# Kernel optimization log

Hardware: AMD Instinct MI355X
Metric: run time of the kernel (lower is better)

## Reference

```python
import jax, jax.numpy as jnp
import numpy as np

EMBED = 768
HEADS = 12
HEAD_DIM = EMBED // HEADS  # 64
NUM_CLS = 1
WIN = 16        # one-sided window radius
DIL = 4         # dilation
THETA = 10000.0
COORD_HIGH = 100000.0


def _rotate_half(x):
    # [..., x1, x2, ...] -> [..., -x2, x1, ...] over adjacent pairs
    x1 = x[..., 0::2]
    x2 = x[..., 1::2]
    return jnp.stack([-x2, x1], axis=-1).reshape(x.shape)


def _rope2d(x, coords):
    # x: (B, H, L, head_dim); coords: (B, L, 2) pixel coords
    half = HEAD_DIM // 2
    inv_freq = 1.0 / THETA ** (jnp.arange(0, half, 2, dtype=jnp.float32) / half)  # (half/2,)
    xy = coords.astype(jnp.float32) / COORD_HIGH
    fx = xy[..., 0:1] * inv_freq  # (B, L, half/2)
    fy = xy[..., 1:2] * inv_freq
    fx = jnp.repeat(fx, 2, axis=-1)  # (B, L, half)
    fy = jnp.repeat(fy, 2, axis=-1)
    freqs = jnp.concatenate([fx, fy], axis=-1)  # (B, L, head_dim)
    cos = jnp.cos(freqs)[:, None]  # (B, 1, L, head_dim)
    sin = jnp.sin(freqs)[:, None]
    return x * cos + _rotate_half(x) * sin


def setup_inputs() -> dict:
    key = jax.random.key(0)
    ks = jax.random.split(key, 5)
    B, L = 1, 4096
    S = L + NUM_CLS
    x = jax.random.normal(ks[0], (B, S, EMBED), jnp.float32)
    coords = jax.random.randint(ks[1], (B, L, 2), 0, 100000).astype(jnp.int32)
    qkv_w = jax.random.normal(ks[2], (3 * EMBED, EMBED), jnp.float32) * 0.02
    qkv_b = jnp.zeros((3 * EMBED,), jnp.float32)
    out_w = jax.random.normal(ks[3], (EMBED, EMBED), jnp.float32) * 0.02
    out_b = jnp.zeros((EMBED,), jnp.float32)
    return {"x": x, "coords": coords, "qkv_w": qkv_w, "qkv_b": qkv_b,
            "out_w": out_w, "out_b": out_b}


def reference(x, coords, qkv_w, qkv_b, out_w, out_b):
    B, S, E = x.shape
    L = S - NUM_CLS
    # QKV projection -> (3, B, H, S, hd)
    qkv = (x @ qkv_w.T + qkv_b).reshape(B, S, 3, HEADS, HEAD_DIM)
    qkv = qkv.transpose(2, 0, 3, 1, 4)
    q, k, v = qkv[0], qkv[1], qkv[2]
    # 2D RoPE on patch tokens only
    q = jnp.concatenate([q[:, :, :NUM_CLS], _rope2d(q[:, :, NUM_CLS:], coords)], axis=2)
    k = jnp.concatenate([k[:, :, :NUM_CLS], _rope2d(k[:, :, NUM_CLS:], coords)], axis=2)
    scale = 1.0 / np.sqrt(HEAD_DIM).astype(np.float32)

    q_cls, k_cls, v_cls = q[:, :, :NUM_CLS], k[:, :, :NUM_CLS], v[:, :, :NUM_CLS]
    q_p, k_p, v_p = q[:, :, NUM_CLS:], k[:, :, NUM_CLS:], v[:, :, NUM_CLS:]

    # CLS (global) queries attend to everything
    cls_scores = jnp.einsum('bhqd,bhkd->bhqk', q_cls, k) * scale
    cls_out = jnp.einsum('bhqk,bhkd->bhqd', jax.nn.softmax(cls_scores, axis=-1), v)

    # Patch queries: single softmax over [CLS keys | dilated local window]
    win_len = 2 * WIN + 1
    pos = jnp.arange(L)
    rel = (jnp.arange(win_len) - WIN) * DIL
    key_idx = pos[:, None] + rel[None, :]          # (L, W) absolute patch key index
    valid = (key_idx >= 0) & (key_idx < L)         # boundary patches: masked, not wrapped
    gidx = jnp.clip(key_idx, 0, L - 1)
    k_win = jnp.take(k_p, gidx, axis=2)            # (B, H, L, W, hd)
    v_win = jnp.take(v_p, gidx, axis=2)
    s_win = jnp.einsum('bhld,bhlwd->bhlw', q_p, k_win) * scale
    s_win = jnp.where(valid[None, None], s_win, -jnp.inf)
    s_cls = jnp.einsum('bhld,bhcd->bhlc', q_p, k_cls) * scale
    attn = jax.nn.softmax(jnp.concatenate([s_cls, s_win], axis=-1), axis=-1)
    a_cls, a_win = attn[..., :NUM_CLS], attn[..., NUM_CLS:]
    patch_out = (jnp.einsum('bhlc,bhcd->bhld', a_cls, v_cls)
                 + jnp.einsum('bhlw,bhlwd->bhld', a_win, v_win))

    out = jnp.concatenate([cls_out, patch_out], axis=2)   # (B, H, S, hd)
    out = out.transpose(0, 2, 1, 3).reshape(B, S, E)
    return out @ out_w.T + out_b
```

## Files before the change

kernel.cpp:

```cpp
#include <hip/hip_runtime.h>
#include <hip/hip_bf16.h>

namespace {

constexpr int kS = 4097;
constexpr int kL = 4096;
constexpr int kE = 768;
constexpr int kH = 12;
constexpr int kD = 64;
constexpr int kQKVN = 2304;
constexpr int kT = 1024;
constexpr int kClsChunks = 32;
constexpr int kClsStride = 68;
constexpr float kScale = 0.125f;

typedef short short8 __attribute__((ext_vector_type(8)));
typedef short short4v __attribute__((ext_vector_type(4)));
typedef float f32x4 __attribute__((ext_vector_type(4)));

__device__ inline short f2bf(float x) {
  __hip_bfloat16 b = __float2bfloat16(x);
  return *reinterpret_cast<short*>(&b);
}
__device__ inline float bf2f(short u) {
  unsigned int x = ((unsigned int)(unsigned short)u) << 16;
  union { unsigned int u32; float f; } c;
  c.u32 = x;
  return c.f;
}

__device__ inline void store_c(float* p, float v) { *p = v; }
__device__ inline void store_c(short* p, float v) { *p = f2bf(v); }

__device__ inline int xcd_swz(int bid, int nwg) {
  const int q = nwg >> 3, r = nwg & 7;
  const int x = bid & 7, o = bid >> 3;
  return (x < r ? x * (q + 1) : r * (q + 1) + (x - r) * q) + o;
}

#define GLOAD_LDS16(g, l)                                                        \
  __builtin_amdgcn_global_load_lds(                                              \
      (const __attribute__((address_space(1))) unsigned int*)(g),                \
      (__attribute__((address_space(3))) unsigned int*)(l), 16, 0, 0)

__global__ __launch_bounds__(256) void cvt3_kernel(const float* __restrict__ x,
                                                   const float* __restrict__ w,
                                                   const float* __restrict__ ow,
                                                   short* __restrict__ xb,
                                                   short* __restrict__ wb,
                                                   short* __restrict__ owb,
                                                   int n4x, int n4w, int n4o) {
  const int total = n4x + n4w + n4o;
  int i = blockIdx.x * blockDim.x + threadIdx.x;
  const int stride = gridDim.x * blockDim.x;
  for (; i < total; i += stride) {
    const float* src;
    short* dst;
    int k;
    if (i < n4x) { src = x; dst = xb; k = i; }
    else if (i < n4x + n4w) { src = w; dst = wb; k = i - n4x; }
    else { src = ow; dst = owb; k = i - n4x - n4w; }
    f32x4 v = reinterpret_cast<const f32x4*>(src)[k];
    short4v o;
#pragma unroll
    for (int j = 0; j < 4; ++j) o[j] = f2bf(v[j]);
    reinterpret_cast<short4v*>(dst)[k] = o;
  }
}

template <bool ROPE, typename TC>
__global__ __launch_bounds__(256) void gemm_tile_kernel(const short* __restrict__ A,
                                                        const short* __restrict__ W,
                                                        const float* __restrict__ bias,
                                                        TC* __restrict__ C,
                                                        int Mreal, int N, int K, int ntm,
                                                        const int* __restrict__ coords) {
  __shared__ short Ash[2][64 * 64];
  __shared__ short Bsh[2][128 * 64];
  const int nwg = gridDim.x;
  const int wid = xcd_swz(blockIdx.x, nwg);
  const int m0 = (wid % ntm) * 64;
  const int n0 = (wid / ntm) * 128;
  const int t = threadIdx.x;
  const int lane = t & 63;
  const int wave = t >> 6;
  const int wr = wave >> 1, wc = wave & 1;
  const int lrow = lane & 15;
  const int lgrp = lane >> 4;

  const int srow = t >> 3;
  const int scol = ((t & 7) ^ (srow & 7)) << 3;
  int ar0 = m0 + srow;       if (ar0 > Mreal - 1) ar0 = Mreal - 1;
  int ar1 = m0 + 32 + srow;  if (ar1 > Mreal - 1) ar1 = Mreal - 1;
  const int br0 = n0 + srow, br1 = n0 + 32 + srow;
  const int br2 = n0 + 64 + srow, br3 = n0 + 96 + srow;

#define STAGE(buf, k0)                                                  \
  do {                                                                  \
    GLOAD_LDS16(A + (size_t)ar0 * K + (k0) + scol, &Ash[buf][t * 8]);   \
    GLOAD_LDS16(A + (size_t)ar1 * K + (k0) + scol, &Ash[buf][2048 + t * 8]); \
    GLOAD_LDS16(W + (size_t)br0 * K + (k0) + scol, &Bsh[buf][t * 8]);   \
    GLOAD_LDS16(W + (size_t)br1 * K + (k0) + scol, &Bsh[buf][2048 + t * 8]); \
    GLOAD_LDS16(W + (size_t)br2 * K + (k0) + scol, &Bsh[buf][4096 + t * 8]); \
    GLOAD_LDS16(W + (size_t)br3 * K + (k0) + scol, &Bsh[buf][6144 + t * 8]); \
  } while (0)

  f32x4 acc[2][4] = {};
  const int nsteps = K / 64;

  STAGE(0, 0);
  __syncthreads();

  int cur = 0;
  for (int tt = 0; tt < nsteps; ++tt) {
    if (tt + 1 < nsteps) STAGE(cur ^ 1, (tt + 1) * 64);

#pragma unroll
    for (int ks = 0; ks < 2; ++ks) {
      short8 a[2], b[4];
#pragma unroll
      for (int mi = 0; mi < 2; ++mi) {
        const int row = wr * 32 + mi * 16 + lrow;
        const int ch = (ks * 4 + lgrp) ^ (row & 7);
        a[mi] = *reinterpret_cast<const short8*>(&Ash[cur][row * 64 + ch * 8]);
      }
#pragma unroll
      for (int ni = 0; ni < 4; ++ni) {
        const int row = wc * 64 + ni * 16 + lrow;
        const int ch = (ks * 4 + lgrp) ^ (row & 7);
        b[ni] = *reinterpret_cast<const short8*>(&Bsh[cur][row * 64 + ch * 8]);
      }
#pragma unroll
      for (int mi = 0; mi < 2; ++mi)
#pragma unroll
        for (int ni = 0; ni < 4; ++ni)
          acc[mi][ni] = __builtin_amdgcn_mfma_f32_16x16x32_bf16(a[mi], b[ni], acc[mi][ni], 0, 0, 0);
    }

    __syncthreads();
    cur ^= 1;
  }
#undef STAGE

  const int rg = lgrp << 2;
  for (int ni = 0; ni < 4; ++ni) {
    const int col = n0 + wc * 64 + ni * 16 + lrow;
    const float bz = bias[col];
    const int sec = col / 768;
    const int dh = col & 63;
    const bool odd = dh & 1;
    const int jf = (dh >> 1) & 15;
    const bool usex = (dh >> 1) < 16;
    const float invf = __powf(10000.0f, -(float)jf * (1.0f / 16.0f));
    for (int mi = 0; mi < 2; ++mi) {
      const int rowb = m0 + wr * 32 + mi * 16 + rg;
#pragma unroll
      for (int r = 0; r < 4; ++r) {
        const int row = rowb + r;
        float v = acc[mi][ni][r] + bz;
        if (ROPE && sec != 2) {
          const float partner = __shfl_xor(v, 1);
          float cs = 1.f, sn = 0.f;
          if (row > 0) {
            const int cl = min(row, kS - 1) - 1;
            const float cx = (float)coords[cl * 2] * 1e-5f;
            const float cy = (float)coords[cl * 2 + 1] * 1e-5f;
            __sincosf((usex ? cx : cy) * invf, &sn, &cs);
          }
          v = odd ? (v * cs + partner * sn) : (v * cs - partner * sn);
          if (sec == 0) v *= kScale;
        }
        if (row < Mreal) store_c(&C[(size_t)row * N + col], v);
      }
    }
  }
}

__global__ __launch_bounds__(256) void attn_kernel(const short* __restrict__ qkv,
                                                   short* __restrict__ attn,
                                                   float* __restrict__ part) {
  __shared__ short Pl[4][32][104];
  __shared__ float sm[4], sl[4], sa[4][64];
  const int lane = threadIdx.x & 63;
  const int wv = threadIdx.x >> 6;

  if (blockIdx.x >= 384) {
    const int idx = blockIdx.x - 384;
    const int h = idx >> 5;
    const int c = idx & 31;
    const int start = c * 128;
    const int end = (c == kClsChunks - 1) ? kS : start + 128;
    const float qd = bf2f(qkv[h * kD + lane]);
    float m = -INFINITY, lsum = 0.f, acc = 0.f;
    for (int s = start + wv; s < end; s += 4) {
      float tt = qd * bf2f(qkv[(size_t)s * kQKVN + kE + h * kD + lane]);
      tt += __shfl_xor(tt, 1); tt += __shfl_xor(tt, 2); tt += __shfl_xor(tt, 4);
      tt += __shfl_xor(tt, 8); tt += __shfl_xor(tt, 16); tt += __shfl_xor(tt, 32);
      const float vd = bf2f(qkv[(size_t)s * kQKVN + 2 * kE + h * kD + lane]);
      const float mnew = fmaxf(m, tt);
      const float cor = __expf(m - mnew);
      const float p = __expf(tt - mnew);
      lsum = lsum * cor + p;
      acc = acc * cor + p * vd;
      m = mnew;
    }
    sa[wv][lane] = acc;
    if (lane == 0) { sm[wv] = m; sl[wv] = lsum; }
    __syncthreads();
    if (wv == 0) {
      float M = fmaxf(fmaxf(sm[0], sm[1]), fmaxf(sm[2], sm[3]));
      float Lt = 0.f, Av = 0.f;
#pragma unroll
      for (int w = 0; w < 4; ++w) {
        const float cw = __expf(sm[w] - M);
        Lt += sl[w] * cw;
        Av += sa[w][lane] * cw;
      }
      float* p = part + ((size_t)h * kClsChunks + c) * kClsStride;
      p[lane] = Av;
      if (lane == 0) { p[64] = M; p[65] = Lt; }
    }
    return;
  }

  const int unit = blockIdx.x * 4 + wv;
  const int t0 = (unit & 31) * 32;
  const int res = (unit >> 5) & 3;
  const int h = unit >> 7;
  const int lrow = lane & 15;
  const int lgrp = lane >> 4;
  const int kg = lgrp * 8;
  const int rg = lgrp * 4;

  f32x4 s_acc[2][4] = {};
  f32x4 s_cls[2] = {};
  short8 aq[2][2];
#pragma unroll
  for (int mi = 0; mi < 2; ++mi) {
    const int tq = t0 + mi * 16 + lrow;
    const size_t row = (size_t)(4 * tq + res + 1) * kQKVN + h * kD;
#pragma unroll
    for (int ks = 0; ks < 2; ++ks)
      aq[mi][ks] = *reinterpret_cast<const short8*>(qkv + row + ks * 32 + kg);
  }
#pragma unroll
  for (int ni = 0; ni < 4; ++ni) {
    int u = t0 - 16 + ni * 16 + lrow;
    u = min(max(u, 0), kT - 1);
    const size_t row = (size_t)(4 * u + res + 1) * kQKVN + kE + h * kD;
    short8 bk[2];
#pragma unroll
    for (int ks = 0; ks < 2; ++ks)
      bk[ks] = *reinterpret_cast<const short8*>(qkv + row + ks * 32 + kg);
#pragma unroll
    for (int mi = 0; mi < 2; ++mi)
#pragma unroll
      for (int ks = 0; ks < 2; ++ks)
        s_acc[mi][ni] = __builtin_amdgcn_mfma_f32_16x16x32_bf16(aq[mi][ks], bk[ks], s_acc[mi][ni], 0, 0, 0);
  }
  {
    short8 bc[2] = {};
    if (lrow == 0) {
#pragma unroll
      for (int ks = 0; ks < 2; ++ks)
        bc[ks] = *reinterpret_cast<const short8*>(qkv + kE + h * kD + ks * 32 + kg);
    }
#pragma unroll
    for (int mi = 0; mi < 2; ++mi)
#pragma unroll
      for (int ks = 0; ks < 2; ++ks)
        s_cls[mi] = __builtin_amdgcn_mfma_f32_16x16x32_bf16(aq[mi][ks], bc[ks], s_cls[mi], 0, 0, 0);
  }

#pragma unroll
  for (int i = 0; i < 2; ++i) {
    const int idx = i * 64 + lane;
    const int q = idx >> 2, ch = idx & 3;
    short8 z = {};
    *reinterpret_cast<short8*>(&Pl[wv][q][64 + ch * 8]) = z;
  }

#pragma unroll
  for (int mi = 0; mi < 2; ++mi) {
#pragma unroll
    for (int r = 0; r < 4; ++r) {
      const int q = mi * 16 + rg + r;
      float sw[4];
      float m = -INFINITY;
#pragma unroll
      for (int ni = 0; ni < 4; ++ni) {
        const int kk = ni * 16 + lrow;
        const int u = t0 - 16 + kk;
        const bool valid = (kk >= q) & (kk <= q + 32) & (u >= 0) & (u < kT);
        sw[ni] = valid ? s_acc[mi][ni][r] : -INFINITY;
        m = fmaxf(m, sw[ni]);
      }
      float scl = (lrow == 0) ? s_cls[mi][r] : -INFINITY;
      m = fmaxf(m, scl);
      m = fmaxf(m, __shfl_xor(m, 1)); m = fmaxf(m, __shfl_xor(m, 2));
      m = fmaxf(m, __shfl_xor(m, 4)); m = fmaxf(m, __shfl_xor(m, 8));
      float lsum = 0.f, ps[4];
#pragma unroll
      for (int ni = 0; ni < 4; ++ni) { ps[ni] = __expf(sw[ni] - m); lsum += ps[ni]; }
      const float pc = __expf(scl - m);
      lsum += pc;
      lsum += __shfl_xor(lsum, 1); lsum += __shfl_xor(lsum, 2);
      lsum += __shfl_xor(lsum, 4); lsum += __shfl_xor(lsum, 8);
      const float inv = __builtin_amdgcn_rcpf(lsum);
#pragma unroll
      for (int ni = 0; ni < 4; ++ni) Pl[wv][q][ni * 16 + lrow] = f2bf(ps[ni] * inv);
      if (lrow == 0) Pl[wv][q][64] = f2bf(pc * inv);
    }
  }

  f32x4 o_acc[4][2] = {};
#pragma unroll
  for (int ks = 0; ks < 3; ++ks) {
    short8 bp[2];
#pragma unroll
    for (int nq = 0; nq < 2; ++nq)
      bp[nq] = *reinterpret_cast<const short8*>(&Pl[wv][nq * 16 + lrow][ks * 32 + kg]);
    short8 av[4];
#pragma unroll
    for (int md = 0; md < 4; ++md) {
      if (ks < 2) {
        const int d = md * 16 + lrow;
#pragma unroll
        for (int e = 0; e < 8; ++e) {
          const int kk = ks * 32 + kg + e;
          int u = t0 - 16 + kk;
          u = min(max(u, 0), kT - 1);
          av[md][e] = qkv[(size_t)(4 * u + res + 1) * kQKVN + 2 * kE + h * kD + d];
        }
      } else {
        short8 z = {};
        av[md] = z;
        if (lgrp == 0)
          av[md][0] = qkv[2 * kE + h * kD + md * 16 + lrow];
      }
#pragma unroll
      for (int nq = 0; nq < 2; ++nq)
        o_acc[md][nq] = __builtin_amdgcn_mfma_f32_16x16x32_bf16(av[md], bp[nq], o_acc[md][nq], 0, 0, 0);
    }
  }

#pragma unroll
  for (int md = 0; md < 4; ++md)
#pragma unroll
    for (int nq = 0; nq < 2; ++nq)
#pragma unroll
      for (int r = 0; r < 4; ++r) {
        const int d = md * 16 + rg + r;
        const int q = nq * 16 + lrow;
        const int s = 4 * (t0 + q) + res + 1;
        attn[(size_t)s * kE + h * kD + d] = f2bf(o_acc[md][nq][r]);
      }
}

__global__ __launch_bounds__(64) void cls_combine_kernel(const float* __restrict__ part,
                                                         short* __restrict__ attn) {
  const int h = blockIdx.x;
  const int lane = threadIdx.x;
  float mc[kClsChunks], lc[kClsChunks], ac[kClsChunks];
#pragma unroll
  for (int c = 0; c < kClsChunks; ++c) {
    const float* p = part + ((size_t)h * kClsChunks + c) * kClsStride;
    mc[c] = p[64];
    lc[c] = p[65];
    ac[c] = p[lane];
  }
  float M = -INFINITY;
#pragma unroll
  for (int c = 0; c < kClsChunks; ++c) M = fmaxf(M, mc[c]);
  float L = 0.f, A = 0.f;
#pragma unroll
  for (int c = 0; c < kClsChunks; ++c) {
    const float w = __expf(mc[c] - M);
    L += lc[c] * w;
    A += ac[c] * w;
  }
  attn[h * kD + lane] = f2bf(A / L);
}

}

extern "C" void kernel_launch(void* const* d_in, const int* in_sizes, int n_in,
                              void* d_out, int out_size, void* d_ws, size_t ws_size,
                              hipStream_t stream) {
  const float* x = (const float*)d_in[0];
  const int* coords = (const int*)d_in[1];
  const float* qkv_w = (const float*)d_in[2];
  const float* qkv_b = (const float*)d_in[3];
  const float* out_w = (const float*)d_in[4];
  const float* out_b = (const float*)d_in[5];
  float* out = (float*)d_out;

  char* p = (char*)d_ws;
  short* qkvb = (short*)p;                p += (size_t)kS * kQKVN * sizeof(short);
  short* xb = (short*)p;                  p += (size_t)kS * kE * sizeof(short);
  short* wb = (short*)p;                  p += (size_t)kQKVN * kE * sizeof(short);
  short* owb = (short*)p;                 p += (size_t)kE * kE * sizeof(short);
  short* attnb = (short*)p;               p += (size_t)kS * kE * sizeof(short);
  float* clsp = (float*)p;

  const int n4x = kS * kE / 4;
  const int n4w = kQKVN * kE / 4;
  const int n4o = kE * kE / 4;
  cvt3_kernel<<<2048, 256, 0, stream>>>(x, qkv_w, out_w, xb, wb, owb, n4x, n4w, n4o);

  gemm_tile_kernel<true, short><<<1170, 256, 0, stream>>>(xb, wb, qkv_b, qkvb, kS, kQKVN, kE, 65, coords);
  attn_kernel<<<768, 256, 0, stream>>>(qkvb, attnb, clsp);
  cls_combine_kernel<<<kH, 64, 0, stream>>>(clsp, attnb);
  gemm_tile_kernel<false, float><<<390, 256, 0, stream>>>(attnb, owb, out_b, out, kS, kE, kE, 65, nullptr);
}
```

Measured before the change: 95.67 us.

## Replace QKV GEMM with 256x256-tile 8-wave kernel using phased LDS pipelining

Adds a new QKV projection GEMM kernel with 256x256 tiles, 512 threads, and double-buffered, split-half LDS staging. It interleaves global-to-LDS loads with MFMA phases under explicit barriers and raised priority. The larger tile increases data reuse and cuts the workgroup count from 1170 to 153. The trade-offs are fewer workgroups than the machine's compute units, padding waste on M, and a heavier RoPE epilogue per thread. The loop count is hard-coded to K=768.

Result: slower. 114.0 us (+19.2%).

```diff
diff --git a/kernel.cpp b/kernel.cpp
--- a/kernel.cpp
+++ b/kernel.cpp
@@ -69,6 +69,185 @@
 }
 
 template <bool ROPE, typename TC>
+__global__ __launch_bounds__(512, 2) void gemm_8ph_kernel(const short* __restrict__ A,
+                                                          const short* __restrict__ W,
+                                                          const float* __restrict__ bias,
+                                                          TC* __restrict__ C,
+                                                          int Mreal, int N, int K, int ntm,
+                                                          const int* __restrict__ coords) {
+  __shared__ short Ash[2][2][128 * 64];
+  __shared__ short Bsh[2][2][128 * 64];
+  const int nwg = gridDim.x;
+  const int wid = xcd_swz(blockIdx.x, nwg);
+  const int m0 = (wid % ntm) * 256;
+  const int n0 = (wid / ntm) * 256;
+  const int t = threadIdx.x;
+  const int lane = t & 63;
+  const int wave = t >> 6;
+  const int wm = wave >> 2;
+  const int wn = wave & 3;
+  const int lrow = lane & 15;
+  const int lgrp = lane >> 4;
+
+  int srow[2], scol[2];
+#pragma unroll
+  for (int j = 0; j < 2; ++j) {
+    const int c = j * 512 + t;
+    srow[j] = c >> 3;
+    scol[j] = ((c & 7) ^ (srow[j] & 7)) << 3;
+  }
+
+#define STAGEA(kt, h)                                                         \
+  do {                                                                        \
+    _Pragma("unroll") for (int j = 0; j < 2; ++j) {                           \
+      int gr = m0 + (h) * 128 + srow[j];                                      \
+      if (gr > Mreal - 1) gr = Mreal - 1;                                     \
+      GLOAD_LDS16(A + (size_t)gr * K + (kt) * 64 + scol[j],                   \
+                  &Ash[(kt) & 1][h][(j * 512 + t) * 8]);                      \
+    }                                                                         \
+  } while (0)
+#define STAGEB(kt, h)                                                         \
+  do {                                                                        \
+    _Pragma("unroll") for (int j = 0; j < 2; ++j) {                           \
+      const int gr = n0 + (h) * 128 + srow[j];                                \
+      GLOAD_LDS16(W + (size_t)gr * K + (kt) * 64 + scol[j],                   \
+                  &Bsh[(kt) & 1][h][(j * 512 + t) * 8]);                      \
+    }                                                                         \
+  } while (0)
+
+  short8 breg[4][2], areg[2][2];
+#define READB(buf)                                                            \
+  do {                                                                        \
+    _Pragma("unroll") for (int nf = 0; nf < 4; ++nf)                          \
+      _Pragma("unroll") for (int ks = 0; ks < 2; ++ks) {                      \
+        const int rowh = (wn & 1) * 64 + nf * 16 + lrow;                      \
+        const int ch = (ks * 4 + lgrp) ^ (rowh & 7);                          \
+        breg[nf][ks] = *reinterpret_cast<const short8*>(                      \
+            &Bsh[buf][wn >> 1][rowh * 64 + ch * 8]);                          \
+      }                                                                       \
+  } while (0)
+#define READA(buf, p)                                                         \
+  do {                                                                        \
+    _Pragma("unroll") for (int mi = 0; mi < 2; ++mi)                          \
+      _Pragma("unroll") for (int ks = 0; ks < 2; ++ks) {                      \
+        const int rowh = ((p) * 2 + mi) * 16 + lrow;                          \
+        const int ch = (ks * 4 + lgrp) ^ (rowh & 7);                          \
+        areg[mi][ks] = *reinterpret_cast<const short8*>(                      \
+            &Ash[buf][wm][rowh * 64 + ch * 8]);                               \
+      }                                                                       \
+  } while (0)
+#define MFMA16(p)                                                             \
+  do {                                                                        \
+    _Pragma("unroll") for (int mi = 0; mi < 2; ++mi)                          \
+      _Pragma("unroll") for (int nf = 0; nf < 4; ++nf)                        \
+        _Pragma("unroll") for (int ks = 0; ks < 2; ++ks)                      \
+          acc[(p) * 2 + mi][nf] = __builtin_amdgcn_mfma_f32_16x16x32_bf16(    \
+              areg[mi][ks], breg[nf][ks], acc[(p) * 2 + mi][nf], 0, 0, 0);    \
+  } while (0)
+#define WAIT_LGKM0                                                            \
+  do {                                                                        \
+    asm volatile("s_waitcnt lgkmcnt(0)" ::: "memory");                        \
+    __builtin_amdgcn_sched_barrier(0);                                        \
+  } while (0)
+#define BAR                                                                   \
+  do {                                                                        \
+    __builtin_amdgcn_sched_barrier(0);                                        \
+    __builtin_amdgcn_s_barrier();                                             \
+    __builtin_amdgcn_sched_barrier(0);                                        \
+  } while (0)
+#define PHASE(buf, p, STAGE_STMT)                                             \
+  do {                                                                        \
+    READA(buf, p);                                                            \
+    STAGE_STMT;                                                               \
+    BAR;                                                                      \
+    WAIT_LGKM0;                                                               \
+    __builtin_amdgcn_s_setprio(1);                                            \
+    MFMA16(p);                                                                \
+    __builtin_amdgcn_s_setprio(0);                                            \
+  } while (0)
+
+  f32x4 acc[8][4] = {};
+
+  STAGEA(0, 0); STAGEA(0, 1); STAGEB(0, 0); STAGEB(0, 1);
+  STAGEB(1, 0); STAGEB(1, 1);
+  asm volatile("s_waitcnt vmcnt(4)" ::: "memory");
+  BAR;
+
+  for (int it = 0; it < 6; ++it) {
+    const int kt1 = 2 * it + 1;
+    const int ktA = 2 * it + 2;
+    const int ktB = 2 * it + 3;
+    const bool more = (it < 5);
+
+    READB(0);
+    PHASE(0, 0, STAGEA(kt1, 0));
+    BAR;
+    PHASE(0, 1, STAGEA(kt1, 1));
+    BAR;
+    PHASE(0, 2, if (more) STAGEB(ktA, 0));
+    BAR;
+    PHASE(0, 3, if (more) STAGEB(ktA, 1));
+    if (more) { asm volatile("s_waitcnt vmcnt(4)" ::: "memory"); }
+    else      { asm volatile("s_waitcnt vmcnt(0)" ::: "memory"); }
+    BAR;
+
+    READB(1);
+    PHASE(1, 0, if (more) STAGEA(ktA, 0));
+    BAR;
+    PHASE(1, 1, if (more) STAGEA(ktA, 1));
+    BAR;
+    PHASE(1, 2, if (more) STAGEB(ktB, 0));
+    BAR;
+    PHASE(1, 3, if (more) STAGEB(ktB, 1));
+    if (more) { asm volatile("s_waitcnt vmcnt(4)" ::: "memory"); }
+    BAR;
+  }
+#undef STAGEA
+#undef STAGEB
+#undef READB
+#undef READA
+#undef MFMA16
+#undef WAIT_LGKM0
+#undef BAR
+#undef PHASE
+
+  const int rg = lgrp << 2;
+#pragma unroll
+  for (int nf = 0; nf < 4; ++nf) {
+    const int col = n0 + wn * 64 + nf * 16 + lrow;
+    const float bz = bias[col];
+    const int sec = col / 768;
+    const int dh = col & 63;
+    const bool odd = dh & 1;
+    const int jf = (dh >> 1) & 15;
+    const bool usex = (dh >> 1) < 16;
+    const float invf = __powf(10000.0f, -(float)jf * (1.0f / 16.0f));
+#pragma unroll
+    for (int mf = 0; mf < 8; ++mf) {
+      const int rowb = m0 + wm * 128 + mf * 16 + rg;
+#pragma unroll
+      for (int r = 0; r < 4; ++r) {
+        const int row = rowb + r;
+        float v = acc[mf][nf][r] + bz;
+        if (ROPE && sec != 2) {
+          const float partner = __shfl_xor(v, 1);
+          float cs = 1.f, sn = 0.f;
+          if (row > 0) {
+            const int cl = min(row, kS - 1) - 1;
+            const float cx = (float)coords[cl * 2] * 1e-5f;
+            const float cy = (float)coords[cl * 2 + 1] * 1e-5f;
+            __sincosf((usex ? cx : cy) * invf, &sn, &cs);
+          }
+          v = odd ? (v * cs + partner * sn) : (v * cs - partner * sn);
+          if (sec == 0) v *= kScale;
+        }
+        if (row < Mreal) store_c(&C[(size_t)row * N + col], v);
+      }
+    }
+  }
+}
+
+template <bool ROPE, typename TC>
 __global__ __launch_bounds__(256) void gemm_tile_kernel(const short* __restrict__ A,
                                                         const short* __restrict__ W,
                                                         const float* __restrict__ bias,
@@ -408,7 +587,7 @@
   const int n4o = kE * kE / 4;
   cvt3_kernel<<<2048, 256, 0, stream>>>(x, qkv_w, out_w, xb, wb, owb, n4x, n4w, n4o);
 
-  gemm_tile_kernel<true, short><<<1170, 256, 0, stream>>>(xb, wb, qkv_b, qkvb, kS, kQKVN, kE, 65, coords);
+  gemm_8ph_kernel<true, short><<<153, 512, 0, stream>>>(xb, wb, qkv_b, qkvb, kS, kQKVN, kE, 17, coords);
   attn_kernel<<<768, 256, 0, stream>>>(qkvb, attnb, clsp);
   cls_combine_kernel<<<kH, 64, 0, stream>>>(clsp, attnb);
   gemm_tile_kernel<false, float><<<390, 256, 0, stream>>>(attnb, owb, out_b, out, kS, kE, kE, 65, nullptr);
```

## Fuse all stages into one persistent kernel with grid barriers and work stealing

Applied to the files above, without the earlier changes.

Replaces the five separate launches (convert, QKV GEMM, attention, CLS combine, output GEMM) with one persistent kernel of 504 blocks. Stages are separated by atomic-counter grid barriers, and tiles within each stage are handed out by an atomic work queue. This removes per-launch overhead and inter-kernel gaps. In exchange it adds barrier spin time and a memset launch. It also risks deadlock if not all blocks are co-resident; a 20M-tick timeout guards against that but could break correctness.

New measurement: 359.8 us. +276.1%, slower.

```diff
diff --git a/kernel.cpp b/kernel.cpp
--- a/kernel.cpp
+++ b/kernel.cpp
@@ -13,6 +13,10 @@
 constexpr int kClsChunks = 32;
 constexpr int kClsStride = 68;
 constexpr float kScale = 0.125f;
+constexpr int kNB = 504;
+constexpr int kG1Tiles = 65 * 18;
+constexpr int kAttnUnits = 768;
+constexpr int kG2Tiles = 65 * 6;
 
 typedef short short8 __attribute__((ext_vector_type(8)));
 typedef short short4v __attribute__((ext_vector_type(4)));
@@ -43,42 +47,32 @@
       (const __attribute__((address_space(1))) unsigned int*)(g),                \
       (__attribute__((address_space(3))) unsigned int*)(l), 16, 0, 0)
 
-__global__ __launch_bounds__(256) void cvt3_kernel(const float* __restrict__ x,
-                                                   const float* __restrict__ w,
-                                                   const float* __restrict__ ow,
-                                                   short* __restrict__ xb,
-                                                   short* __restrict__ wb,
-                                                   short* __restrict__ owb,
-                                                   int n4x, int n4w, int n4o) {
-  const int total = n4x + n4w + n4o;
-  int i = blockIdx.x * blockDim.x + threadIdx.x;
-  const int stride = gridDim.x * blockDim.x;
-  for (; i < total; i += stride) {
-    const float* src;
-    short* dst;
-    int k;
-    if (i < n4x) { src = x; dst = xb; k = i; }
-    else if (i < n4x + n4w) { src = w; dst = wb; k = i - n4x; }
-    else { src = ow; dst = owb; k = i - n4x - n4w; }
-    f32x4 v = reinterpret_cast<const f32x4*>(src)[k];
-    short4v o;
-#pragma unroll
-    for (int j = 0; j < 4; ++j) o[j] = f2bf(v[j]);
-    reinterpret_cast<short4v*>(dst)[k] = o;
-  }
+__device__ inline void gsync(unsigned* bar, unsigned nblk) {
+  __syncthreads();
+  if (threadIdx.x == 0) {
+    __threadfence();
+    atomicAdd(bar, 1u);
+    const long long t0 = (long long)__builtin_amdgcn_s_memrealtime();
+    while (atomicAdd(bar, 0u) < nblk) {
+      __builtin_amdgcn_s_sleep(8);
+      if ((long long)__builtin_amdgcn_s_memrealtime() - t0 > 20000000ll) break;
+    }
+    __threadfence();
+  }
+  __syncthreads();
 }
 
 template <bool ROPE, typename TC>
-__global__ __launch_bounds__(256) void gemm_tile_kernel(const short* __restrict__ A,
-                                                        const short* __restrict__ W,
-                                                        const float* __restrict__ bias,
-                                                        TC* __restrict__ C,
-                                                        int Mreal, int N, int K, int ntm,
-                                                        const int* __restrict__ coords) {
-  __shared__ short Ash[2][64 * 64];
-  __shared__ short Bsh[2][128 * 64];
-  const int nwg = gridDim.x;
-  const int wid = xcd_swz(blockIdx.x, nwg);
+__device__ __forceinline__ void gemm_tile(short* ldsA, short* ldsB,
+                                          const short* __restrict__ A,
+                                          const short* __restrict__ W,
+                                          const float* __restrict__ bias,
+                                          TC* __restrict__ C,
+                                          int Mreal, int N, int K, int ntm, int vb, int nvb,
+                                          const int* __restrict__ coords) {
+  short (*Ash)[64 * 64] = reinterpret_cast<short (*)[64 * 64]>(ldsA);
+  short (*Bsh)[128 * 64] = reinterpret_cast<short (*)[128 * 64]>(ldsB);
+  const int wid = xcd_swz(vb, nvb);
   const int m0 = (wid % ntm) * 64;
   const int n0 = (wid / ntm) * 128;
   const int t = threadIdx.x;
@@ -176,16 +170,19 @@
   }
 }
 
-__global__ __launch_bounds__(256) void attn_kernel(const short* __restrict__ qkv,
-                                                   short* __restrict__ attn,
-                                                   float* __restrict__ part) {
-  __shared__ short Pl[4][32][104];
-  __shared__ float sm[4], sl[4], sa[4][64];
+__device__ __forceinline__ void attn_unit(char* lds, int vb,
+                                          const short* __restrict__ qkv,
+                                          short* __restrict__ attn,
+                                          float* __restrict__ part) {
+  short (*Pl)[32][104] = reinterpret_cast<short (*)[32][104]>(lds);
+  float* sm = reinterpret_cast<float*>(lds + 26624);
+  float* sl = reinterpret_cast<float*>(lds + 26688);
+  float (*sa)[64] = reinterpret_cast<float (*)[64]>(lds + 26752);
   const int lane = threadIdx.x & 63;
   const int wv = threadIdx.x >> 6;
 
-  if (blockIdx.x >= 384) {
-    const int idx = blockIdx.x - 384;
+  if (vb >= 384) {
+    const int idx = vb - 384;
     const int h = idx >> 5;
     const int c = idx & 31;
     const int start = c * 128;
@@ -223,7 +220,7 @@
     return;
   }
 
-  const int unit = blockIdx.x * 4 + wv;
+  const int unit = vb * 4 + wv;
   const int t0 = (unit & 31) * 32;
   const int res = (unit >> 5) & 3;
   const int h = unit >> 7;
@@ -357,29 +354,96 @@
       }
 }
 
-__global__ __launch_bounds__(64) void cls_combine_kernel(const float* __restrict__ part,
-                                                         short* __restrict__ attn) {
-  const int h = blockIdx.x;
-  const int lane = threadIdx.x;
-  float mc[kClsChunks], lc[kClsChunks], ac[kClsChunks];
-#pragma unroll
-  for (int c = 0; c < kClsChunks; ++c) {
-    const float* p = part + ((size_t)h * kClsChunks + c) * kClsStride;
-    mc[c] = p[64];
-    lc[c] = p[65];
-    ac[c] = p[lane];
-  }
-  float M = -INFINITY;
-#pragma unroll
-  for (int c = 0; c < kClsChunks; ++c) M = fmaxf(M, mc[c]);
-  float L = 0.f, A = 0.f;
-#pragma unroll
-  for (int c = 0; c < kClsChunks; ++c) {
-    const float w = __expf(mc[c] - M);
-    L += lc[c] * w;
-    A += ac[c] * w;
-  }
-  attn[h * kD + lane] = f2bf(A / L);
+__global__ __launch_bounds__(256, 2) void fused_kernel(
+    const float* __restrict__ x, const int* __restrict__ coords,
+    const float* __restrict__ qkv_w, const float* __restrict__ qkv_b,
+    const float* __restrict__ out_w, const float* __restrict__ out_b,
+    float* __restrict__ out,
+    short* __restrict__ xb, short* __restrict__ wb, short* __restrict__ owb,
+    short* __restrict__ qkvb, short* __restrict__ attnb,
+    float* __restrict__ clsp, unsigned* __restrict__ ctrl) {
+  __shared__ alignas(16) char lds[49152];
+  __shared__ unsigned vb_sh;
+  const unsigned nblk = gridDim.x;
+  short* ldsA = reinterpret_cast<short*>(lds);
+  short* ldsB = reinterpret_cast<short*>(lds + 16384);
+
+  {
+    const int n4x = kS * kE / 4, n4w = kQKVN * kE / 4, n4o = kE * kE / 4;
+    const int total = n4x + n4w + n4o;
+    const int stride = nblk * 256;
+    for (int i = blockIdx.x * 256 + threadIdx.x; i < total; i += stride) {
+      const float* src;
+      short* dst;
+      int k;
+      if (i < n4x) { src = x; dst = xb; k = i; }
+      else if (i < n4x + n4w) { src = qkv_w; dst = wb; k = i - n4x; }
+      else { src = out_w; dst = owb; k = i - n4x - n4w; }
+      f32x4 v = reinterpret_cast<const f32x4*>(src)[k];
+      short4v o;
+#pragma unroll
+      for (int j = 0; j < 4; ++j) o[j] = f2bf(v[j]);
+      reinterpret_cast<short4v*>(dst)[k] = o;
+    }
+  }
+  gsync(&ctrl[0], nblk);
+
+  for (;;) {
+    if (threadIdx.x == 0) vb_sh = atomicAdd(&ctrl[4], 1u);
+    __syncthreads();
+    const unsigned vb = vb_sh;
+    __syncthreads();
+    if (vb >= kG1Tiles) break;
+    gemm_tile<true, short>(ldsA, ldsB, xb, wb, qkv_b, qkvb, kS, kQKVN, kE, 65,
+                           (int)vb, kG1Tiles, coords);
+  }
+  gsync(&ctrl[1], nblk);
+
+  for (;;) {
+    if (threadIdx.x == 0) vb_sh = atomicAdd(&ctrl[5], 1u);
+    __syncthreads();
+    const unsigned vb = vb_sh;
+    __syncthreads();
+    if (vb >= kAttnUnits) break;
+    attn_unit(lds, (int)vb, qkvb, attnb, clsp);
+    __syncthreads();
+  }
+  gsync(&ctrl[2], nblk);
+
+  if (blockIdx.x < kH && threadIdx.x < 64) {
+    const int h = blockIdx.x;
+    const int lane = threadIdx.x;
+    float mc[kClsChunks], lc[kClsChunks], ac[kClsChunks];
+#pragma unroll
+    for (int c = 0; c < kClsChunks; ++c) {
+      const float* pp = clsp + ((size_t)h * kClsChunks + c) * kClsStride;
+      mc[c] = pp[64];
+      lc[c] = pp[65];
+      ac[c] = pp[lane];
+    }
+    float M = -INFINITY;
+#pragma unroll
+    for (int c = 0; c < kClsChunks; ++c) M = fmaxf(M, mc[c]);
+    float L = 0.f, Av = 0.f;
+#pragma unroll
+    for (int c = 0; c < kClsChunks; ++c) {
+      const float w = __expf(mc[c] - M);
+      L += lc[c] * w;
+      Av += ac[c] * w;
+    }
+    attnb[h * kD + lane] = f2bf(Av / L);
+  }
+  gsync(&ctrl[3], nblk);
+
+  for (;;) {
+    if (threadIdx.x == 0) vb_sh = atomicAdd(&ctrl[6], 1u);
+    __syncthreads();
+    const unsigned vb = vb_sh;
+    __syncthreads();
+    if (vb >= kG2Tiles) break;
+    gemm_tile<false, float>(ldsA, ldsB, attnb, owb, out_b, out, kS, kE, kE, 65,
+                            (int)vb, kG2Tiles, nullptr);
+  }
 }
 
 }
@@ -401,15 +465,11 @@
   short* wb = (short*)p;                  p += (size_t)kQKVN * kE * sizeof(short);
   short* owb = (short*)p;                 p += (size_t)kE * kE * sizeof(short);
   short* attnb = (short*)p;               p += (size_t)kS * kE * sizeof(short);
-  float* clsp = (float*)p;
-
-  const int n4x = kS * kE / 4;
-  const int n4w = kQKVN * kE / 4;
-  const int n4o = kE * kE / 4;
-  cvt3_kernel<<<2048, 256, 0, stream>>>(x, qkv_w, out_w, xb, wb, owb, n4x, n4w, n4o);
-
-  gemm_tile_kernel<true, short><<<1170, 256, 0, stream>>>(xb, wb, qkv_b, qkvb, kS, kQKVN, kE, 65, coords);
-  attn_kernel<<<768, 256, 0, stream>>>(qkvb, attnb, clsp);
-  cls_combine_kernel<<<kH, 64, 0, stream>>>(clsp, attnb);
-  gemm_tile_kernel<false, float><<<390, 256, 0, stream>>>(attnb, owb, out_b, out, kS, kE, kE, 65, nullptr);
-}
+  float* clsp = (float*)p;                p += (size_t)kH * kClsChunks * kClsStride * sizeof(float);
+  p = (char*)(((uintptr_t)p + 255) & ~(uintptr_t)255);
+  unsigned* ctrl = (unsigned*)p;
+
+  hipMemsetAsync(ctrl, 0, 64, stream);
+  fused_kernel<<<kNB, 256, 0, stream>>>(x, coords, qkv_w, qkv_b, out_w, out_b, out,
+                                        xb, wb, owb, qkvb, attnb, clsp, ctrl);
+}
```
